# Performance work log

Measured on AMD Instinct MI355X. Metric: run time of the kernel, lower is better.

## Reference

```python
import jax, jax.numpy as jnp
import numpy as np

B, L = 2, 4096
D_MODEL = 1024
EXPAND = 2
D_INNER = EXPAND * D_MODEL            # 2048
HEADDIM = 64
NHEADS = D_INNER // HEADDIM           # 32
D_STATE = 128
NGROUPS = 1
D_CONV = 4
D_OUT = 1024
D_IN_PROJ = 2 * D_INNER + 2 * NGROUPS * D_STATE + NHEADS  # 4384
CONV_DIM = D_INNER + 2 * NGROUPS * D_STATE                # 2304
EPS = 1e-5


def setup_inputs() -> dict:
    key = jax.random.key(0)
    ks = jax.random.split(key, 8)
    x = jax.random.normal(ks[0], (B, L, D_MODEL), jnp.float32)
    in_proj_w = jax.random.normal(ks[1], (D_IN_PROJ, D_MODEL), jnp.float32) * (1.0 / np.sqrt(D_MODEL))
    conv_w = jax.random.normal(ks[2], (CONV_DIM, D_CONV), jnp.float32) * (1.0 / np.sqrt(D_CONV))
    conv_b = jnp.zeros((CONV_DIM,), jnp.float32)
    # dt_bias init as in the module: inverse-softplus of dt ~ LogUniform(1e-3, 1e-1)
    dt = jnp.exp(jax.random.uniform(ks[3], (NHEADS,)) * (np.log(0.1) - np.log(0.001)) + np.log(0.001))
    dt_bias = dt + jnp.log(-jnp.expm1(-dt))
    A_log = jnp.log(jax.random.uniform(ks[4], (NHEADS,), minval=1.0, maxval=16.0))
    Dp = jnp.ones((NHEADS,), jnp.float32)
    norm_w = jnp.ones((D_INNER,), jnp.float32)
    out_proj_w = jax.random.normal(ks[5], (D_OUT, D_INNER), jnp.float32) * (1.0 / np.sqrt(D_INNER))
    return {"x": x, "in_proj_w": in_proj_w, "conv_w": conv_w, "conv_b": conv_b,
            "dt_bias": dt_bias, "A_log": A_log, "Dp": Dp, "norm_w": norm_w,
            "out_proj_w": out_proj_w}


def _mamba_fwd(x, in_proj_w, conv_w, conv_b, dt_bias, A_log, Dp, norm_w, out_proj_w):
    # in_proj (no bias): (B,L,D_MODEL) -> (B,L,D_IN_PROJ)
    zxbcdt = jnp.einsum('bld,ed->ble', x, in_proj_w)
    z = zxbcdt[..., :D_INNER]                                  # gate branch
    xBC = zxbcdt[..., D_INNER:D_INNER + CONV_DIM]              # conv branch
    dt = zxbcdt[..., D_INNER + CONV_DIM:]                      # (B,L,H)
    # depthwise causal conv1d + SiLU
    xBC_t = jnp.transpose(xBC, (0, 2, 1))                      # (B, C, L)
    conv_out = jax.lax.conv_general_dilated(
        xBC_t, conv_w[:, None, :], window_strides=(1,),
        padding=[(D_CONV - 1, 0)],
        dimension_numbers=('NCH', 'OIH', 'NCH'),
        feature_group_count=CONV_DIM)
    xBC = jax.nn.silu(jnp.transpose(conv_out + conv_b[None, :, None], (0, 2, 1)))
    xs = xBC[..., :D_INNER].reshape(B, L, NHEADS, HEADDIM)     # (B,L,H,P)
    Bm = xBC[..., D_INNER:D_INNER + D_STATE]                   # (B,L,N), ngroups=1
    Cm = xBC[..., D_INNER + D_STATE:]                          # (B,L,N)
    A = -jnp.exp(A_log)                                        # (H,)
    dt = jax.nn.softplus(dt + dt_bias)                         # (B,L,H)
    dA = jnp.exp(dt * A)                                       # (B,L,H)

    def step(h, inp):
        dA_t, dt_t, B_t, x_t, C_t = inp
        # h: (B,H,P,N) selective state-space recurrence
        h = h * dA_t[:, :, None, None] + jnp.einsum('bh,bn,bhp->bhpn', dt_t, B_t, x_t)
        y = jnp.einsum('bhpn,bn->bhp', h, C_t)
        return h, y

    h0 = jnp.zeros((B, NHEADS, HEADDIM, D_STATE), xs.dtype)
    _, ys = jax.lax.scan(step, h0,
                         (jnp.swapaxes(dA, 0, 1), jnp.swapaxes(dt, 0, 1),
                          jnp.swapaxes(Bm, 0, 1), jnp.swapaxes(xs, 0, 1),
                          jnp.swapaxes(Cm, 0, 1)))
    y = jnp.swapaxes(ys, 0, 1) + Dp[None, None, :, None] * xs  # skip term D*x
    y = y.reshape(B, L, D_INNER)
    # gated RMSNorm (norm_before_gate=False): norm(y * silu(z)) * w
    y = y * jax.nn.silu(z)
    y = y * jax.lax.rsqrt(jnp.mean(y * y, axis=-1, keepdims=True) + EPS) * norm_w
    return jnp.einsum('bld,od->blo', y, out_proj_w)


def reference(x, in_proj_w, conv_w, conv_b, dt_bias, A_log, Dp, norm_w, out_proj_w):
    return _mamba_fwd(x, in_proj_w, conv_w, conv_b, dt_bias, A_log, Dp, norm_w, out_proj_w)
```

## Files before the change

### kernel.cpp

```cpp
#include <hip/hip_runtime.h>

#define LL 4096
#define DMODEL 1024
#define DINNER 2048
#define NHEADS 32
#define DSTATE 128
#define DINPROJ 4384
#define NZX 4352
#define CONVDIM 2304
#define ROWS 8192
#define Q 64
#define NCS 64
#define XCSEQ ((size_t)LL*CONVDIM)
#define LGSEQ ((size_t)NHEADS*NCS*Q)

typedef __attribute__((ext_vector_type(8))) __bf16 bf16x8;
typedef __attribute__((ext_vector_type(4))) float f32x4;

__device__ __forceinline__ float bf2f(ushort u){ union{uint i;float f;} v; v.i=(uint)u<<16; return v.f; }
__device__ __forceinline__ ushort f2bf(float f){ union{float f;uint i;} v; v.f=f; uint r=v.i+0x7fffu+((v.i>>16)&1u); return (ushort)(r>>16); }

__global__ __launch_bounds__(256) void cvt_all(
    const float4* __restrict__ x, uint4* __restrict__ xbf,
    const float4* __restrict__ ipw, ushort4* __restrict__ Wp,
    const float4* __restrict__ opw, uint4* __restrict__ opwb){
  int b = blockIdx.x, tid = threadIdx.x;
  if (b < 4096){
    long t = (long)b*256 + tid;
    float4 a = x[t*2], bb = x[t*2+1];
    ushort u[8] = { f2bf(a.x),f2bf(a.y),f2bf(a.z),f2bf(a.w),
                    f2bf(bb.x),f2bf(bb.y),f2bf(bb.z),f2bf(bb.w) };
    xbf[t] = *(uint4*)u;
  } else if (b < 4096 + 4480){
    int row = b - 4096;
    ushort4 o = make_ushort4(0,0,0,0);
    if (row < DINPROJ){
      float4 f = ipw[(size_t)row*256 + tid];
      o = make_ushort4(f2bf(f.x), f2bf(f.y), f2bf(f.z), f2bf(f.w));
    }
    Wp[(size_t)row*256 + tid] = o;
  } else {
    long t = (long)(b - 8576)*256 + tid;
    float4 a = opw[t*2], bb = opw[t*2+1];
    ushort u[8] = { f2bf(a.x),f2bf(a.y),f2bf(a.z),f2bf(a.w),
                    f2bf(bb.x),f2bf(bb.y),f2bf(bb.z),f2bf(bb.w) };
    opwb[t] = *(uint4*)u;
  }
}

__device__ __forceinline__ void gld16(const void* g, void* l){
  __builtin_amdgcn_global_load_lds((const __attribute__((address_space(1))) void*)g,
                                   (__attribute__((address_space(3))) void*)l, 16, 0, 0);
}

#define GBM 128
#define GBN 128
#define GBK 32

__global__ __launch_bounds__(256) void gemm_tile(
    const ushort* __restrict__ A, int lda, long grow0, long rowmax,
    const ushort* __restrict__ W, int ldw,
    void* __restrict__ Cv, int ldc, int K, int obf, int swz, int q, int r,
    float* __restrict__ Cdt){
  __shared__ __align__(16) ushort As[2][GBM*GBK];
  __shared__ __align__(16) ushort Bs[2][GBN*GBK];
  const int tid = threadIdx.x;
  const int lane = tid & 63, wave = tid >> 6;
  const int wm = wave >> 1, wn = wave & 1;
  int bx, by;
  if (swz){
    int wgid = blockIdx.y * gridDim.x + blockIdx.x;
    int xcd = wgid & 7, i = wgid >> 3;
    int vid = (xcd < r) ? xcd*(q+1) + i : r*(q+1) + (xcd - r)*q + i;
    int rows = gridDim.y;
    if (((rows & 7) == 0) && (r == 0)){
      int rp = rows >> 3;
      int lv = vid - xcd*q;
      by = xcd*rp + (lv % rp);
      bx = lv / rp;
    } else { by = vid / (int)gridDim.x; bx = vid % (int)gridDim.x; }
  } else { bx = blockIdx.x; by = blockIdx.y; }
  const int m0 = by * GBM, n0 = bx * GBN;

  const int srow = lane >> 2;
  const int scol = (((lane & 3) ^ ((lane >> 3) & 3)) * 8);
  long ra0 = grow0 + m0 + 16*wave + srow;      if (ra0 < 0) ra0 = 0; if (ra0 > rowmax) ra0 = rowmax;
  long ra1 = grow0 + m0 + 64 + 16*wave + srow; if (ra1 < 0) ra1 = 0; if (ra1 > rowmax) ra1 = rowmax;
  const ushort* gA0 = A + ra0*(long)lda + scol;
  const ushort* gA1 = A + ra1*(long)lda + scol;
  const ushort* gB0 = W + (size_t)(n0 + 16*wave + srow)*ldw + scol;
  const ushort* gB1 = W + (size_t)(n0 + 64 + 16*wave + srow)*ldw + scol;
  ushort* lA0 = &As[0][0] + (16*wave)*GBK;
  ushort* lA1 = &As[0][0] + (64 + 16*wave)*GBK;
  ushort* lB0 = &Bs[0][0] + (16*wave)*GBK;
  ushort* lB1 = &Bs[0][0] + (64 + 16*wave)*GBK;

  const int fr = lane & 15, quad = lane >> 4;
  const int es = ((quad ^ ((fr >> 1) & 3)) * 8);
  f32x4 acc[4][4] = {};

#define STAGE(buf, ko) { \
    gld16(gA0 + (ko), lA0 + (buf)*(GBM*GBK)); \
    gld16(gA1 + (ko), lA1 + (buf)*(GBM*GBK)); \
    gld16(gB0 + (ko), lB0 + (buf)*(GBN*GBK)); \
    gld16(gB1 + (ko), lB1 + (buf)*(GBN*GBK)); }

  STAGE(0, 0);
  __syncthreads();
  int cur = 0;
  const int nst = K / GBK;
  for (int s = 0; s < nst; ++s){
    if (s + 1 < nst) STAGE(cur^1, (s+1)*GBK);
    const ushort* Ab = &As[cur][0];
    const ushort* Bb = &Bs[cur][0];
    bf16x8 af[4], bw[4];
    #pragma unroll
    for (int i=0;i<4;i++) af[i] = *(const bf16x8*)(Ab + (wm*64 + i*16 + fr)*GBK + es);
    #pragma unroll
    for (int j=0;j<4;j++) bw[j] = *(const bf16x8*)(Bb + (wn*64 + j*16 + fr)*GBK + es);
    #pragma unroll
    for (int i=0;i<4;i++)
      #pragma unroll
      for (int j=0;j<4;j++)
        acc[i][j] = __builtin_amdgcn_mfma_f32_16x16x32_bf16(af[i], bw[j], acc[i][j], 0,0,0);
    if (s + 1 < nst){ __syncthreads(); cur ^= 1; }
  }
#undef STAGE
  if (Cdt && n0 >= NZX){
    int nb = n0 - NZX;
    #pragma unroll
    for (int i=0;i<4;i++)
      #pragma unroll
      for (int j=0;j<4;j++){
        size_t base = (size_t)(m0 + wm*64 + i*16 + quad*4)*128 + (nb + wn*64 + j*16 + fr);
        #pragma unroll
        for (int rr=0;rr<4;rr++)
          Cdt[base + (size_t)rr*128] = acc[i][j][rr];
      }
  } else if (obf){
    ushort* Cb = (ushort*)Cv;
    #pragma unroll
    for (int i=0;i<4;i++)
      #pragma unroll
      for (int j=0;j<4;j++){
        size_t base = (size_t)(m0 + wm*64 + i*16 + quad*4)*ldc + (n0 + wn*64 + j*16 + fr);
        #pragma unroll
        for (int rr=0;rr<4;rr++)
          Cb[base + (size_t)rr*ldc] = f2bf(acc[i][j][rr]);
      }
  } else {
    float* Cf = (float*)Cv;
    #pragma unroll
    for (int i=0;i<4;i++)
      #pragma unroll
      for (int j=0;j<4;j++){
        size_t base = (size_t)(m0 + wm*64 + i*16 + quad*4)*ldc + (n0 + wn*64 + j*16 + fr);
        #pragma unroll
        for (int rr=0;rr<4;rr++)
          Cf[base + (size_t)rr*ldc] = acc[i][j][rr];
      }
  }
}

__global__ __launch_bounds__(256) void conv8(const ushort* __restrict__ zxh,
    const float* __restrict__ cw, const float* __restrict__ cb,
    ushort* __restrict__ xconv, int l0, long base){
  int z = blockIdx.y;
  long bb = base + (long)z*LL;
  ushort* xc = xconv + (size_t)z*XCSEQ;
  int id = blockIdx.x*256 + threadIdx.x;
  int g = id % 288, band = id / 288;
  int c = g*8;
  float w[8][4], bias[8];
  #pragma unroll
  for (int i=0;i<8;i++){
    bias[i] = cb[c+i];
    #pragma unroll
    for (int j=0;j<4;j++) w[i][j] = cw[(c+i)*4+j];
  }
  float in[7][8];
  #pragma unroll
  for (int k=0;k<7;k++){
    int lrow = l0 + band*4 - 3 + k;
    if (lrow < 0){
      #pragma unroll
      for (int i=0;i<8;i++) in[k][i] = 0.f;
    } else {
      uint4 v = *(const uint4*)(zxh + (size_t)(bb + band*4 - 3 + k)*NZX + DINNER + c);
      const ushort* us = (const ushort*)&v;
      #pragma unroll
      for (int i=0;i<8;i++) in[k][i] = bf2f(us[i]);
    }
  }
  #pragma unroll
  for (int r=0;r<4;r++){
    ushort o[8];
    #pragma unroll
    for (int i=0;i<8;i++){
      float a = bias[i];
      #pragma unroll
      for (int j=0;j<4;j++) a = fmaf(in[r+j][i], w[i][j], a);
      float v = a / (1.f + expf(-a));
      o[i] = f2bf(v);
    }
    *(uint4*)(xc + (size_t)(band*4 + r)*CONVDIM + c) = *(uint4*)o;
  }
}

__global__ __launch_bounds__(256) void scan_pre2(const ushort* __restrict__ xcv0,
    const float* __restrict__ dtraw, long dtrow0,
    const float* __restrict__ dtb, const float* __restrict__ alog,
    ushort* __restrict__ gbuf0, ushort* __restrict__ gbuf1,
    float* __restrict__ lgbuf0, int cslot0){
  const int c = blockIdx.x, h = blockIdx.y, z = blockIdx.z;
  const ushort* xcv = xcv0 + (size_t)z*XCSEQ;
  const long dtr0 = dtrow0 + (long)z*LL;
  ushort* gbuf = z ? gbuf1 : gbuf0;
  float* lgbuf = lgbuf0 + (size_t)z*LGSEQ;
  const int cslot = cslot0 + c;
  const int tid = threadIdx.x, lane = tid & 63, w = tid >> 6;
  const int l15 = lane & 15, quad = lane >> 4, kq = quad*8;
  __shared__ float wsx[Q];
  __shared__ __align__(16) ushort XT[64*72];
  __shared__ __align__(16) ushort BTw[128*72];
  const int c0 = c*Q;
  if (tid < 64){
    float xv = dtraw[(size_t)(dtr0 + c0 + tid)*128 + h] + dtb[h];
    float sp = (xv > 20.f) ? xv : log1pf(expf(xv));
    float la = sp * (-expf(alog[h]));
    float v = la;
    #pragma unroll
    for (int off=1; off<64; off<<=1){ float u = __shfl_up(v, off); if (tid >= off) v += u; }
    float tot = __shfl(v, 63);
    wsx[tid] = __expf(tot - v)*sp;
    lgbuf[((size_t)h*NCS + cslot)*Q + tid] = v;
  }
  __syncthreads();
  { int s = tid>>2, pb = (tid&3)*16;
    const ushort* src = xcv + (size_t)(c0+s)*CONVDIM + h*64 + pb;
    ushort tmp[16];
    *(uint4*)tmp     = *(const uint4*)src;
    *(uint4*)(tmp+8) = *(const uint4*)(src+8);
    #pragma unroll
    for (int i=0;i<16;i++) XT[(pb+i)*72 + s] = tmp[i];
  }
  { int s = tid>>2, nb4 = (tid&3)*32;
    const ushort* src = xcv + (size_t)(c0+s)*CONVDIM + DINNER + nb4;
    float wv = wsx[s];
    ushort tmp[32];
    #pragma unroll
    for (int v4=0;v4<4;v4++) *(uint4*)(tmp+v4*8) = *(const uint4*)(src+v4*8);
    #pragma unroll
    for (int i=0;i<32;i++) BTw[(nb4+i)*72 + s] = f2bf(bf2f(tmp[i])*wv);
  }
  __syncthreads();
  f32x4 g[8] = {};
  #pragma unroll
  for (int kb=0;kb<2;kb++){
    bf16x8 afr = *(const bf16x8*)(XT + (16*w + l15)*72 + kb*32 + kq);
    #pragma unroll
    for (int j=0;j<8;j++){
      bf16x8 bfr = *(const bf16x8*)(BTw + (16*j + l15)*72 + kb*32 + kq);
      g[j] = __builtin_amdgcn_mfma_f32_16x16x32_bf16(afr, bfr, g[j], 0,0,0);
    }
  }
  __syncthreads();
  ushort* gst = &BTw[0];
  #pragma unroll
  for (int j=0;j<8;j++)
    #pragma unroll
    for (int r=0;r<4;r++)
      gst[(16*w + quad*4 + r)*136 + 16*j + l15] = f2bf(g[j][r]);
  __syncthreads();
  { int row = tid >> 2, seg = tid & 3;
    const ushort* gs = gst + row*136 + seg*32;
    uint4 a = *(const uint4*)(gs);
    uint4 b = *(const uint4*)(gs + 8);
    uint4 c2 = *(const uint4*)(gs + 16);
    uint4 d = *(const uint4*)(gs + 24);
    ushort* gdst = gbuf + ((size_t)h*NCS + cslot)*8192 + row*128 + seg*32;
    *(uint4*)gdst = a;
    *(uint4*)(gdst + 8) = b;
    *(uint4*)(gdst + 16) = c2;
    *(uint4*)(gdst + 24) = d;
  }
}

__global__ __launch_bounds__(256) void scan_carry2(ushort* __restrict__ g0p,
    ushort* __restrict__ g1p, const float* __restrict__ lgbuf0, int ncs){
  const int qtr = blockIdx.x, h = blockIdx.y, z = blockIdx.z;
  ushort* gh = z ? g1p : g0p;
  const float* lgbuf = lgbuf0 + (size_t)z*LGSEQ;
  const int tid = threadIdx.x;
  __shared__ float es[NCS];
  if (tid < ncs) es[tid] = __expf(lgbuf[((size_t)h*NCS + tid)*Q + 63]);
  __syncthreads();
  float hreg[8] = {0.f,0.f,0.f,0.f,0.f,0.f,0.f,0.f};
  ushort* p0 = gh + (size_t)h*NCS*8192 + qtr*2048 + tid*8;
  uint4 g0 = *(const uint4*)p0;
  uint4 g1 = *(const uint4*)(p0 + 8192);
  for (int c = 0; c < ncs; ++c){
    ushort* pc = p0 + (size_t)c*8192;
    uint4 gc = g0; g0 = g1;
    if (c + 2 < ncs) g1 = *(const uint4*)(pc + 2*8192);
    ushort u[8];
    #pragma unroll
    for (int i=0;i<8;i++) u[i] = f2bf(hreg[i]);
    *(uint4*)pc = *(uint4*)u;
    float e = es[c];
    const ushort* gs = (const ushort*)&gc;
    #pragma unroll
    for (int i=0;i<8;i++) hreg[i] = fmaf(hreg[i], e, bf2f(gs[i]));
  }
}

__global__ __launch_bounds__(256) void scan_y2(ushort* __restrict__ xcv0,
    const float* __restrict__ dtraw, long dtrow0,
    const float* __restrict__ dtb, const float* __restrict__ alog,
    const float* __restrict__ lgbuf0, const ushort* __restrict__ gbuf0,
    const ushort* __restrict__ gbuf1, const float* __restrict__ Dp, int cslot0){
  const int c = blockIdx.x, h = blockIdx.y, z = blockIdx.z;
  ushort* xcv = xcv0 + (size_t)z*XCSEQ;
  const long dtr0 = dtrow0 + (long)z*LL;
  const ushort* gbuf = z ? gbuf1 : gbuf0;
  const float* lgbuf = lgbuf0 + (size_t)z*LGSEQ;
  const int cslot = cslot0 + c;
  const int tid = threadIdx.x, lane = tid & 63, w = tid >> 6;
  const int l15 = lane & 15, quad = lane >> 4, kq = quad*8;
  __shared__ float lg[Q], dts[Q], els[Q];
  __shared__ __align__(16) ushort XT[64*72];
  __shared__ __align__(16) ushort Cc[64*136];
  __shared__ __align__(16) ushort Bp[64*136];
  const int c0 = c*Q;
  if (tid < 64){
    float v = lgbuf[((size_t)h*NCS + cslot)*Q + tid];
    lg[tid] = v;
    els[tid] = __expf(v);
    float xv = dtraw[(size_t)(dtr0 + c0 + tid)*128 + h] + dtb[h];
    dts[tid] = (xv > 20.f) ? xv : log1pf(expf(xv));
  }
  { int s = tid>>2, pb = (tid&3)*16;
    const ushort* src = xcv + (size_t)(c0+s)*CONVDIM + h*64 + pb;
    ushort tmp[16];
    *(uint4*)tmp     = *(const uint4*)src;
    *(uint4*)(tmp+8) = *(const uint4*)(src+8);
    #pragma unroll
    for (int i=0;i<16;i++) XT[(pb+i)*72 + s] = tmp[i];
  }
  { int row = tid >> 2, seg = tid & 3;
    const ushort* bsrc = xcv + (size_t)(c0 + row)*CONVDIM + DINNER + seg*32;
    const ushort* csrc = bsrc + DSTATE;
    #pragma unroll
    for (int k=0;k<4;k++){
      *(uint4*)(Bp + row*136 + seg*32 + k*8) = *(const uint4*)(bsrc + k*8);
      *(uint4*)(Cc + row*136 + seg*32 + k*8) = *(const uint4*)(csrc + k*8);
    }
  }
  __syncthreads();
  f32x4 sac[4] = {};
  #pragma unroll
  for (int kb=0;kb<4;kb++){
    bf16x8 afr = *(const bf16x8*)(Cc + (16*w + l15)*136 + kb*32 + kq);
    #pragma unroll
    for (int j=0;j<4;j++){
      bf16x8 bfr = *(const bf16x8*)(Bp + (16*j + l15)*136 + kb*32 + kq);
      sac[j] = __builtin_amdgcn_mfma_f32_16x16x32_bf16(afr, bfr, sac[j], 0,0,0);
    }
  }
  __syncthreads();
  #pragma unroll
  for (int j=0;j<4;j++){
    int s = 16*j + l15;
    float lgs = lg[s], dtss = dts[s];
    #pragma unroll
    for (int r=0;r<4;r++){
      int t = 16*w + quad*4 + r;
      float val = (t >= s) ? sac[j][r]*__expf(lg[t]-lgs)*dtss : 0.f;
      Bp[t*72 + s] = f2bf(val);
    }
  }
  __syncthreads();
  float yv[4][4];
  {
    const float dph = Dp[h];
    bf16x8 hb[4], xb[2];
    const ushort* hrow = gbuf + ((size_t)h*NCS + cslot)*8192 + (16*w + l15)*128;
    #pragma unroll
    for (int kb=0;kb<4;kb++) hb[kb] = *(const bf16x8*)(hrow + kb*32 + kq);
    #pragma unroll
    for (int kb=0;kb<2;kb++) xb[kb] = *(const bf16x8*)(XT + (16*w + l15)*72 + kb*32 + kq);
    #pragma unroll
    for (int i=0;i<4;i++){
      f32x4 y2 = {};
      #pragma unroll
      for (int kb=0;kb<4;kb++){
        bf16x8 afr = *(const bf16x8*)(Cc + (16*i + l15)*136 + kb*32 + kq);
        y2 = __builtin_amdgcn_mfma_f32_16x16x32_bf16(afr, hb[kb], y2, 0,0,0);
      }
      f32x4 y1 = {};
      #pragma unroll
      for (int kb=0;kb<2;kb++){
        bf16x8 afr = *(const bf16x8*)(Bp + (16*i + l15)*72 + kb*32 + kq);
        y1 = __builtin_amdgcn_mfma_f32_16x16x32_bf16(afr, xb[kb], y1, 0,0,0);
      }
      int p = 16*w + l15;
      #pragma unroll
      for (int r=0;r<4;r++){
        int t = 16*i + quad*4 + r;
        float xv = bf2f(XT[p*72 + t]);
        yv[i][r] = y1[r] + els[t]*y2[r] + dph*xv;
      }
    }
  }
  __syncthreads();
  {
    int p = 16*w + l15;
    #pragma unroll
    for (int i=0;i<4;i++)
      #pragma unroll
      for (int r=0;r<4;r++)
        Bp[(16*i + quad*4 + r)*72 + p] = f2bf(yv[i][r]);
  }
  __syncthreads();
  { int t = tid >> 2, seg = tid & 3;
    uint4 a = *(const uint4*)(Bp + t*72 + seg*16);
    uint4 b = *(const uint4*)(Bp + t*72 + seg*16 + 8);
    ushort* od = xcv + (size_t)(c0 + t)*CONVDIM + h*64 + seg*16;
    *(uint4*)od = a;
    *(uint4*)(od + 8) = b;
  }
}

__global__ __launch_bounds__(256) void gate_norm2(const ushort* __restrict__ ybase0,
    const ushort* __restrict__ zbase0, ushort* __restrict__ obase0,
    const float* __restrict__ nw){
  int lr = blockIdx.x, z = blockIdx.y, tid = threadIdx.x;
  const ushort* ybase = ybase0 + (size_t)z*XCSEQ;
  const ushort* zbase = zbase0 + (size_t)z*LL*NZX;
  ushort* obase = obase0 + (size_t)z*LL*NZX;
  int d0 = tid*8;
  const ushort* yrow = ybase + (size_t)lr*CONVDIM;
  const ushort* zrow = zbase + (size_t)lr*NZX;
  uint4 yu = *(const uint4*)(yrow + d0);
  uint4 zu = *(const uint4*)(zrow + d0);
  const ushort* yus = (const ushort*)&yu;
  const ushort* zus = (const ushort*)&zu;
  float y[8]; float ss = 0.f;
  #pragma unroll
  for (int i=0;i<8;i++){
    float zz = bf2f(zus[i]);
    float g = zz / (1.f + expf(-zz));
    float v = bf2f(yus[i]) * g;
    y[i] = v; ss += v*v;
  }
  #pragma unroll
  for (int m=1;m<64;m<<=1) ss += __shfl_xor(ss, m);
  __shared__ float red[4];
  if ((tid & 63) == 0) red[tid>>6] = ss;
  __syncthreads();
  ss = red[0]+red[1]+red[2]+red[3];
  float scale = rsqrtf(ss * (1.f/DINNER) + 1e-5f);
  ushort o[8];
  #pragma unroll
  for (int i=0;i<8;i++)
    o[i] = f2bf(y[i] * scale * nw[d0+i]);
  *(uint4*)(obase + (size_t)lr*NZX + d0) = *(uint4*)o;
}

extern "C" void kernel_launch(void* const* d_in, const int* in_sizes, int n_in,
                              void* d_out, int out_size, void* d_ws, size_t ws_size,
                              hipStream_t stream) {
  const float* x    = (const float*)d_in[0];
  const float* ipw  = (const float*)d_in[1];
  const float* cw   = (const float*)d_in[2];
  const float* cb   = (const float*)d_in[3];
  const float* dtb  = (const float*)d_in[4];
  const float* alog = (const float*)d_in[5];
  const float* Dp   = (const float*)d_in[6];
  const float* nw   = (const float*)d_in[7];
  const float* opw  = (const float*)d_in[8];
  char* ws = (char*)d_ws;
  size_t off = 0;
  ushort* Wp    = (ushort*)(ws + off); off += (size_t)4480*DMODEL*2;
  ushort* opwb  = (ushort*)(ws + off); off += (size_t)DMODEL*DINNER*2;
  float*  dtraw = (float*)(ws + off);  off += (size_t)ROWS*128*4;
  ushort* zxbh  = (ushort*)(ws + off); off += (size_t)ROWS*NZX*2;

  const size_t lg_b  = LGSEQ*4;
  const size_t xc_b  = XCSEQ*2;
  const size_t xc_fb = (size_t)1024*CONVDIM*2;
  const size_t gb_b  = (size_t)NHEADS*NCS*8192*2;

  size_t needA = off + 2*lg_b + 2*xc_b + gb_b;
  size_t needB = off + lg_b + xc_b + gb_b;
  int mode = (ws_size >= needA) ? 2 : (ws_size >= needB ? 1 : 0);

  float* lgbuf = (float*)(ws + off); off += (mode == 2) ? 2*lg_b : lg_b;
  ushort* xconv = (ushort*)(ws + off);
  off += (mode == 2) ? 2*xc_b : (mode == 1 ? xc_b : xc_fb);
  ushort* xbf  = (ushort*)(ws + off);
  ushort* gbuf0 = (ushort*)(ws + off);
  ushort* gbuf1 = (mode == 2) ? (ushort*)d_out : gbuf0;

  cvt_all<<<9600, 256, 0, stream>>>((const float4*)x, (uint4*)xbf,
                                    (const float4*)ipw, (ushort4*)Wp,
                                    (const float4*)opw, (uint4*)opwb);

  gemm_tile<<<dim3(35, 64), 256, 0, stream>>>(
      xbf, DMODEL, 0, (long)ROWS-1, Wp, DMODEL,
      zxbh, NZX, DMODEL, 1, 1, 280, 0, dtraw);

  if (mode == 2){
    conv8<<<dim3(288*(LL/4)/256, 2), 256, 0, stream>>>(zxbh, cw, cb, xconv, 0, 0);
    scan_pre2<<<dim3(NCS, NHEADS, 2), 256, 0, stream>>>(
        xconv, dtraw, 0, dtb, alog, gbuf0, gbuf1, lgbuf, 0);
    scan_carry2<<<dim3(4, NHEADS, 2), 256, 0, stream>>>(gbuf0, gbuf1, lgbuf, NCS);
    scan_y2<<<dim3(NCS, NHEADS, 2), 256, 0, stream>>>(
        xconv, dtraw, 0, dtb, alog, lgbuf, gbuf0, gbuf1, Dp, 0);
    gate_norm2<<<dim3(LL, 2), 256, 0, stream>>>(xconv, zxbh, zxbh + DINNER, nw);
  } else if (mode == 1){
    for (int b = 0; b < 2; ++b){
      long row0 = (long)b*LL;
      conv8<<<dim3(288*(LL/4)/256, 1), 256, 0, stream>>>(zxbh, cw, cb, xconv, 0, row0);
      scan_pre2<<<dim3(NCS, NHEADS, 1), 256, 0, stream>>>(
          xconv, dtraw, row0, dtb, alog, gbuf0, gbuf0, lgbuf, 0);
      scan_carry2<<<dim3(4, NHEADS, 1), 256, 0, stream>>>(gbuf0, gbuf0, lgbuf, NCS);
      scan_y2<<<dim3(NCS, NHEADS, 1), 256, 0, stream>>>(
          xconv, dtraw, row0, dtb, alog, lgbuf, gbuf0, gbuf0, Dp, 0);
      gate_norm2<<<dim3(LL, 1), 256, 0, stream>>>(
          xconv, zxbh + (size_t)row0*NZX, zxbh + (size_t)row0*NZX + DINNER, nw);
    }
  } else {
    for (int b = 0; b < 2; ++b){
      long row0 = (long)b*LL;
      for (int ckl = 0; ckl < 4; ++ckl){
        long g0 = row0 + (long)ckl*1024;
        conv8<<<dim3(288*(1024/4)/256, 1), 256, 0, stream>>>(zxbh, cw, cb, xconv, ckl*1024, g0);
        scan_pre2<<<dim3(16, NHEADS, 1), 256, 0, stream>>>(
            xconv, dtraw, g0, dtb, alog, gbuf0, gbuf0, lgbuf, ckl*16);
      }
      scan_carry2<<<dim3(4, NHEADS, 1), 256, 0, stream>>>(gbuf0, gbuf0, lgbuf, NCS);
      for (int ckl = 0; ckl < 4; ++ckl){
        long g0 = row0 + (long)ckl*1024;
        scan_y2<<<dim3(16, NHEADS, 1), 256, 0, stream>>>(
            xconv, dtraw, g0, dtb, alog, lgbuf, gbuf0, gbuf0, Dp, ckl*16);
        gate_norm2<<<dim3(1024, 1), 256, 0, stream>>>(
            xconv, zxbh + (size_t)g0*NZX, zxbh + (size_t)g0*NZX + DINNER, nw);
      }
    }
  }

  gemm_tile<<<dim3(8, 64), 256, 0, stream>>>(
      zxbh + DINNER, NZX, 0, (long)ROWS-1, opwb, DINNER,
      (float*)d_out, DMODEL, DINNER, 0, 1, 64, 0, nullptr);
}
```

Before: 389.0 us.

## Fuse gated RMSNorm into scan epilogue and out-projection GEMM

Removes the separate gate_norm2 kernel. The SiLU(z) gate is applied inside scan_y2, which also writes per-head sums of squares into spare columns of the dt buffer. norm_w is folded into the bf16 out-projection weights at conversion time. The out-projection GEMM then reads the gated y directly from xconv, computes each row's rsqrt scale from the 32 head partial sums, and applies it to the accumulators. This drops one full read/write pass of the activations and one launch, at the cost of strided z loads in the scan and extra prologue work in the GEMM.

After: 384.0 us. Within noise of the previous version (-1.3%).

```diff
diff --git a/kernel.cpp b/kernel.cpp
--- a/kernel.cpp
+++ b/kernel.cpp
@@ -23,7 +23,8 @@
 __global__ __launch_bounds__(256) void cvt_all(
     const float4* __restrict__ x, uint4* __restrict__ xbf,
     const float4* __restrict__ ipw, ushort4* __restrict__ Wp,
-    const float4* __restrict__ opw, uint4* __restrict__ opwb){
+    const float4* __restrict__ opw, uint4* __restrict__ opwb,
+    const float* __restrict__ nw){
   int b = blockIdx.x, tid = threadIdx.x;
   if (b < 4096){
     long t = (long)b*256 + tid;
@@ -42,8 +43,11 @@
   } else {
     long t = (long)(b - 8576)*256 + tid;
     float4 a = opw[t*2], bb = opw[t*2+1];
-    ushort u[8] = { f2bf(a.x),f2bf(a.y),f2bf(a.z),f2bf(a.w),
-                    f2bf(bb.x),f2bf(bb.y),f2bf(bb.z),f2bf(bb.w) };
+    long e0 = t*8;
+    float w0 = nw[(e0+0)&2047], w1 = nw[(e0+1)&2047], w2 = nw[(e0+2)&2047], w3 = nw[(e0+3)&2047];
+    float w4 = nw[(e0+4)&2047], w5 = nw[(e0+5)&2047], w6 = nw[(e0+6)&2047], w7 = nw[(e0+7)&2047];
+    ushort u[8] = { f2bf(a.x*w0),f2bf(a.y*w1),f2bf(a.z*w2),f2bf(a.w*w3),
+                    f2bf(bb.x*w4),f2bf(bb.y*w5),f2bf(bb.z*w6),f2bf(bb.w*w7) };
     opwb[t] = *(uint4*)u;
   }
 }
@@ -61,9 +65,10 @@
     const ushort* __restrict__ A, int lda, long grow0, long rowmax,
     const ushort* __restrict__ W, int ldw,
     void* __restrict__ Cv, int ldc, int K, int obf, int swz, int q, int r,
-    float* __restrict__ Cdt){
+    float* __restrict__ Cdt, const float* __restrict__ rowsc){
   __shared__ __align__(16) ushort As[2][GBM*GBK];
   __shared__ __align__(16) ushort Bs[2][GBN*GBK];
+  __shared__ float scl[128];
   const int tid = threadIdx.x;
   const int lane = tid & 63, wave = tid >> 6;
   const int wm = wave >> 1, wn = wave & 1;
@@ -106,6 +111,14 @@
     gld16(gB1 + (ko), lB1 + (buf)*(GBN*GBK)); }
 
   STAGE(0, 0);
+  if (rowsc && tid < 128){
+    long rr = grow0 + m0 + tid; if (rr < 0) rr = 0; if (rr > rowmax) rr = rowmax;
+    const float* pr = rowsc + (size_t)rr*128;
+    float s = 0.f;
+    #pragma unroll
+    for (int h=0;h<32;h++) s += pr[h];
+    scl[tid] = rsqrtf(s*(1.f/(float)DINNER) + 1e-5f);
+  }
   __syncthreads();
   int cur = 0;
   const int nst = K / GBK;
@@ -126,6 +139,17 @@
     if (s + 1 < nst){ __syncthreads(); cur ^= 1; }
   }
 #undef STAGE
+  if (rowsc){
+    #pragma unroll
+    for (int i=0;i<4;i++){
+      #pragma unroll
+      for (int rr=0;rr<4;rr++){
+        float sv = scl[wm*64 + i*16 + quad*4 + rr];
+        #pragma unroll
+        for (int j=0;j<4;j++) acc[i][j][rr] *= sv;
+      }
+    }
+  }
   if (Cdt && n0 >= NZX){
     int nb = n0 - NZX;
     #pragma unroll
@@ -315,7 +339,8 @@
 }
 
 __global__ __launch_bounds__(256) void scan_y2(ushort* __restrict__ xcv0,
-    const float* __restrict__ dtraw, long dtrow0,
+    const ushort* __restrict__ zxh,
+    float* __restrict__ dtraw, long dtrow0,
     const float* __restrict__ dtb, const float* __restrict__ alog,
     const float* __restrict__ lgbuf0, const ushort* __restrict__ gbuf0,
     const ushort* __restrict__ gbuf1, const float* __restrict__ Dp, int cslot0){
@@ -412,6 +437,17 @@
       }
     }
   }
+  {
+    const ushort* zcol = zxh + (size_t)(dtr0 + c0)*NZX + h*64 + (16*w + l15);
+    #pragma unroll
+    for (int i=0;i<4;i++)
+      #pragma unroll
+      for (int r=0;r<4;r++){
+        int t = 16*i + quad*4 + r;
+        float zz = bf2f(zcol[(size_t)t*NZX]);
+        yv[i][r] *= zz / (1.f + expf(-zz));
+      }
+  }
   __syncthreads();
   {
     int p = 16*w + l15;
@@ -428,43 +464,16 @@
     ushort* od = xcv + (size_t)(c0 + t)*CONVDIM + h*64 + seg*16;
     *(uint4*)od = a;
     *(uint4*)(od + 8) = b;
-  }
-}
-
-__global__ __launch_bounds__(256) void gate_norm2(const ushort* __restrict__ ybase0,
-    const ushort* __restrict__ zbase0, ushort* __restrict__ obase0,
-    const float* __restrict__ nw){
-  int lr = blockIdx.x, z = blockIdx.y, tid = threadIdx.x;
-  const ushort* ybase = ybase0 + (size_t)z*XCSEQ;
-  const ushort* zbase = zbase0 + (size_t)z*LL*NZX;
-  ushort* obase = obase0 + (size_t)z*LL*NZX;
-  int d0 = tid*8;
-  const ushort* yrow = ybase + (size_t)lr*CONVDIM;
-  const ushort* zrow = zbase + (size_t)lr*NZX;
-  uint4 yu = *(const uint4*)(yrow + d0);
-  uint4 zu = *(const uint4*)(zrow + d0);
-  const ushort* yus = (const ushort*)&yu;
-  const ushort* zus = (const ushort*)&zu;
-  float y[8]; float ss = 0.f;
-  #pragma unroll
-  for (int i=0;i<8;i++){
-    float zz = bf2f(zus[i]);
-    float g = zz / (1.f + expf(-zz));
-    float v = bf2f(yus[i]) * g;
-    y[i] = v; ss += v*v;
-  }
-  #pragma unroll
-  for (int m=1;m<64;m<<=1) ss += __shfl_xor(ss, m);
-  __shared__ float red[4];
-  if ((tid & 63) == 0) red[tid>>6] = ss;
-  __syncthreads();
-  ss = red[0]+red[1]+red[2]+red[3];
-  float scale = rsqrtf(ss * (1.f/DINNER) + 1e-5f);
-  ushort o[8];
-  #pragma unroll
-  for (int i=0;i<8;i++)
-    o[i] = f2bf(y[i] * scale * nw[d0+i]);
-  *(uint4*)(obase + (size_t)lr*NZX + d0) = *(uint4*)o;
+    const ushort* ya = (const ushort*)&a;
+    const ushort* yb2 = (const ushort*)&b;
+    float ss = 0.f;
+    #pragma unroll
+    for (int i=0;i<8;i++){ float v1 = bf2f(ya[i]); float v2 = bf2f(yb2[i]); ss = fmaf(v1,v1, fmaf(v2,v2, ss)); }
+    ss += __shfl_xor(ss, 1);
+    ss += __shfl_xor(ss, 2);
+    if (seg == 0)
+      dtraw[(size_t)(dtr0 + c0 + t)*128 + 64 + h] = ss;
+  }
 }
 
 extern "C" void kernel_launch(void* const* d_in, const int* in_sizes, int n_in,
@@ -504,11 +513,11 @@
 
   cvt_all<<<9600, 256, 0, stream>>>((const float4*)x, (uint4*)xbf,
                                     (const float4*)ipw, (ushort4*)Wp,
-                                    (const float4*)opw, (uint4*)opwb);
+                                    (const float4*)opw, (uint4*)opwb, nw);
 
   gemm_tile<<<dim3(35, 64), 256, 0, stream>>>(
       xbf, DMODEL, 0, (long)ROWS-1, Wp, DMODEL,
-      zxbh, NZX, DMODEL, 1, 1, 280, 0, dtraw);
+      zxbh, NZX, DMODEL, 1, 1, 280, 0, dtraw, nullptr);
 
   if (mode == 2){
     conv8<<<dim3(288*(LL/4)/256, 2), 256, 0, stream>>>(zxbh, cw, cb, xconv, 0, 0);
@@ -516,8 +525,10 @@
         xconv, dtraw, 0, dtb, alog, gbuf0, gbuf1, lgbuf, 0);
     scan_carry2<<<dim3(4, NHEADS, 2), 256, 0, stream>>>(gbuf0, gbuf1, lgbuf, NCS);
     scan_y2<<<dim3(NCS, NHEADS, 2), 256, 0, stream>>>(
-        xconv, dtraw, 0, dtb, alog, lgbuf, gbuf0, gbuf1, Dp, 0);
-    gate_norm2<<<dim3(LL, 2), 256, 0, stream>>>(xconv, zxbh, zxbh + DINNER, nw);
+        xconv, zxbh, dtraw, 0, dtb, alog, lgbuf, gbuf0, gbuf1, Dp, 0);
+    gemm_tile<<<dim3(8, 64), 256, 0, stream>>>(
+        xconv, CONVDIM, 0, (long)ROWS-1, opwb, DINNER,
+        (float*)d_out, DMODEL, DINNER, 0, 1, 64, 0, nullptr, dtraw + 64);
   } else if (mode == 1){
     for (int b = 0; b < 2; ++b){
       long row0 = (long)b*LL;
@@ -526,9 +537,11 @@
           xconv, dtraw, row0, dtb, alog, gbuf0, gbuf0, lgbuf, 0);
       scan_carry2<<<dim3(4, NHEADS, 1), 256, 0, stream>>>(gbuf0, gbuf0, lgbuf, NCS);
       scan_y2<<<dim3(NCS, NHEADS, 1), 256, 0, stream>>>(
-          xconv, dtraw, row0, dtb, alog, lgbuf, gbuf0, gbuf0, Dp, 0);
-      gate_norm2<<<dim3(LL, 1), 256, 0, stream>>>(
-          xconv, zxbh + (size_t)row0*NZX, zxbh + (size_t)row0*NZX + DINNER, nw);
+          xconv, zxbh, dtraw, row0, dtb, alog, lgbuf, gbuf0, gbuf0, Dp, 0);
+      gemm_tile<<<dim3(8, 32), 256, 0, stream>>>(
+          xconv, CONVDIM, 0, (long)LL-1, opwb, DINNER,
+          (float*)d_out + (size_t)row0*DMODEL, DMODEL, DINNER, 0, 1, 32, 0,
+          nullptr, dtraw + 64 + (size_t)row0*128);
     }
   } else {
     for (int b = 0; b < 2; ++b){
@@ -542,15 +555,14 @@
       scan_carry2<<<dim3(4, NHEADS, 1), 256, 0, stream>>>(gbuf0, gbuf0, lgbuf, NCS);
       for (int ckl = 0; ckl < 4; ++ckl){
         long g0 = row0 + (long)ckl*1024;
+        conv8<<<dim3(288*(1024/4)/256, 1), 256, 0, stream>>>(zxbh, cw, cb, xconv, ckl*1024, g0);
         scan_y2<<<dim3(16, NHEADS, 1), 256, 0, stream>>>(
-            xconv, dtraw, g0, dtb, alog, lgbuf, gbuf0, gbuf0, Dp, ckl*16);
-        gate_norm2<<<dim3(1024, 1), 256, 0, stream>>>(
-            xconv, zxbh + (size_t)g0*NZX, zxbh + (size_t)g0*NZX + DINNER, nw);
-      }
-    }
-  }
-
-  gemm_tile<<<dim3(8, 64), 256, 0, stream>>>(
-      zxbh + DINNER, NZX, 0, (long)ROWS-1, opwb, DINNER,
-      (float*)d_out, DMODEL, DINNER, 0, 1, 64, 0, nullptr);
-}
+            xconv, zxbh, dtraw, g0, dtb, alog, lgbuf, gbuf0, gbuf0, Dp, ckl*16);
+        gemm_tile<<<dim3(8, 8), 256, 0, stream>>>(
+            xconv, CONVDIM, 0, 1023L, opwb, DINNER,
+            (float*)d_out + (size_t)g0*DMODEL, DMODEL, DINNER, 0, 1, 8, 0,
+            nullptr, dtraw + 64 + (size_t)g0*128);
+      }
+    }
+  }
+}
```
